# Kernel tuning notes

Measured on AMD Instinct MI355X. Metric: run time of the kernel, lower is better.

## Reference

```python
import jax, jax.numpy as jnp
import numpy as np

N_NODES = 50000
N_EDGES = 800000
IN_DIM = 128
ADD = 8
HIDDEN = 256
OUT_DIM = 128


def gcn_conv(x, src, dst, W, b, n_nodes):
    """PyG GCNConv: linear -> sym-normalized scatter-add with self-loops -> bias."""
    loop = jnp.arange(n_nodes, dtype=src.dtype)
    s = jnp.concatenate([src, loop])
    d = jnp.concatenate([dst, loop])
    deg = jax.ops.segment_sum(jnp.ones(s.shape[0], dtype=x.dtype), d, num_segments=n_nodes)
    dinv = jnp.where(deg > 0, jax.lax.rsqrt(deg), 0.0)
    norm = dinv[s] * dinv[d]                       # [E+N]
    h = x @ W                                      # [N, F_out]
    msg = h[s] * norm[:, None]                     # [E+N, F_out]
    out = jax.ops.segment_sum(msg, d, num_segments=n_nodes)
    return out + b


def prelu(x, a):
    return jnp.where(x >= 0, x, a * x)


def setup_inputs() -> dict:
    key = jax.random.key(0)
    ks = jax.random.split(key, 8)
    x = jax.random.normal(ks[0], (N_NODES, IN_DIM), dtype=jnp.float32)
    edge_index = jax.random.randint(ks[1], (2, N_EDGES), 0, N_NODES, dtype=jnp.int64)
    id_vec = jax.random.normal(ks[2], (ADD,), dtype=jnp.float32)
    # Glorot-ish init for linear weights, PReLU slope 0.25 (torch default)
    W1 = jax.random.normal(ks[3], (IN_DIM + ADD, HIDDEN), dtype=jnp.float32) * 0.05
    b1 = jnp.zeros((HIDDEN,), dtype=jnp.float32)
    a1 = jnp.full((HIDDEN,), 0.25, dtype=jnp.float32)
    W2 = jax.random.normal(ks[4], (HIDDEN, OUT_DIM), dtype=jnp.float32) * 0.05
    b2 = jnp.zeros((OUT_DIM,), dtype=jnp.float32)
    a2 = jnp.full((OUT_DIM,), 0.25, dtype=jnp.float32)
    return {"x": x, "edge_index": edge_index, "id": id_vec,
            "W1": W1, "b1": b1, "a1": a1, "W2": W2, "b2": b2, "a2": a2}


def reference(x, edge_index, id, W1, b1, a1, W2, b2, a2):
    n = x.shape[0]
    src, dst = edge_index[0], edge_index[1]
    # tile id vector onto every node and concat along features
    xi = jnp.concatenate([x, jnp.broadcast_to(id[None, :], (n, id.shape[0]))], axis=1)
    h = gcn_conv(xi, src, dst, W1, b1, n)
    h = prelu(h, a1)
    h = gcn_conv(h, src, dst, W2, b2, n)
    h = prelu(h, a2)
    return h
```

## Files before the change

kernel.cpp:

```cpp
#include <hip/hip_runtime.h>


constexpr int NN = 50000;
constexpr int NE = 800000;
constexpr int NBUCK = 98;
constexpr int TILE = 8192;
constexpr int NSCAT = (NE + TILE - 1) / TILE;

typedef __attribute__((ext_vector_type(8))) short short8;
typedef __attribute__((ext_vector_type(4))) float floatx4;

__device__ inline void bsplit(float v, unsigned short& hi, unsigned short& lo) {
  unsigned u = __float_as_uint(v);
  hi = (unsigned short)(u >> 16);
  float rem = v - __uint_as_float(u & 0xffff0000u);
  lo = (unsigned short)(__float_as_uint(rem) >> 16);
}

__device__ inline unsigned short bf16_rtne(float v) {
  unsigned u = __float_as_uint(v);
  return (unsigned short)((u + 0x7fffu + ((u >> 16) & 1u)) >> 16);
}

__device__ inline float bflo(unsigned u) { return __uint_as_float(u << 16); }
__device__ inline float bfhi(unsigned u) { return __uint_as_float(u & 0xffff0000u); }


__global__ void zero_small_kernel(int* __restrict__ bcnt) {
  int t = threadIdx.x;
  if (t < NBUCK) bcnt[t] = 0;
}

__global__ __launch_bounds__(256) void bucket_count_kernel(const int* __restrict__ ei,
                                                           int* __restrict__ bcnt) {
  __shared__ int h[NBUCK];
  int t = threadIdx.x;
  for (int i = t; i < NBUCK; i += 256) h[i] = 0;
  __syncthreads();
  int base = blockIdx.x * TILE;
  int end = base + TILE; if (end > NE) end = NE;
  for (int e = base + t; e < end; e += 256) {
    int d = ei[NE + e];
    atomicAdd(&h[d >> 9], 1);
  }
  __syncthreads();
  for (int i = t; i < NBUCK; i += 256)
    if (h[i]) atomicAdd(&bcnt[i], h[i]);
}

__global__ void bucket_scan_kernel(const int* __restrict__ bcnt, int* __restrict__ bbase,
                                   int* __restrict__ bcur) {
  __shared__ int sm[128];
  int t = threadIdx.x;
  int v = (t < NBUCK) ? bcnt[t] : 0;
  sm[t] = v;
  __syncthreads();
  for (int off = 1; off < 128; off <<= 1) {
    int u = (t >= off) ? sm[t - off] : 0;
    __syncthreads();
    sm[t] += u;
    __syncthreads();
  }
  if (t < NBUCK) {
    bbase[t] = sm[t] - v;
    bcur[t] = sm[t] - v;
  }
}

__global__ __launch_bounds__(256) void bucket_scatter_kernel(const int* __restrict__ ei,
                                                             int* __restrict__ bcur,
                                                             unsigned* __restrict__ ebuf) {
  __shared__ int h[NBUCK], lbase[NBUCK], gb[NBUCK], lcur[NBUCK];
  __shared__ int ssc[128];
  __shared__ unsigned stage[TILE];
  int t = threadIdx.x;
  for (int i = t; i < NBUCK; i += 256) h[i] = 0;
  __syncthreads();
  int base = blockIdx.x * TILE;
  int end = base + TILE; if (end > NE) end = NE;
  for (int e = base + t; e < end; e += 256) {
    int d = ei[NE + e];
    atomicAdd(&h[d >> 9], 1);
  }
  __syncthreads();
  if (t < 128) ssc[t] = (t < NBUCK) ? h[t] : 0;
  __syncthreads();
  for (int off = 1; off < 128; off <<= 1) {
    int u = 0;
    if (t < 128 && t >= off) u = ssc[t - off];
    __syncthreads();
    if (t < 128) ssc[t] += u;
    __syncthreads();
  }
  if (t < NBUCK) {
    int ex = ssc[t] - h[t];
    lbase[t] = ex;
    lcur[t] = ex;
    gb[t] = atomicAdd(&bcur[t], h[t]);
  }
  __syncthreads();
  for (int e = base + t; e < end; e += 256) {
    int s = ei[e];
    int d = ei[NE + e];
    int b = d >> 9;
    int pos = atomicAdd(&lcur[b], 1);
    stage[pos] = ((unsigned)(d & 511) << 16) | (unsigned)s;
  }
  __syncthreads();
  for (int b = 0; b < NBUCK; ++b) {
    int c = h[b], lb = lbase[b], g = gb[b];
    for (int i = t; i < c; i += 256) ebuf[g + i] = stage[lb + i];
  }
}

__global__ __launch_bounds__(256) void bucket_csr_kernel(
    const unsigned* __restrict__ ebuf, const int* __restrict__ bbase,
    const int* __restrict__ bcnt, int* __restrict__ offs, int* __restrict__ col,
    float* __restrict__ dinv) {
  __shared__ int cnt[512], cur[512], sums[256];
  int b = blockIdx.x, t = threadIdx.x;
  int node0 = b << 9;
  int nnode = NN - node0; if (nnode > 512) nnode = 512;
  for (int i = t; i < 512; i += 256) cnt[i] = 0;
  __syncthreads();
  int g0 = bbase[b], g1 = g0 + bcnt[b];
  for (int i = g0 + t; i < g1; i += 256) atomicAdd(&cnt[ebuf[i] >> 16], 1);
  __syncthreads();
  int c0 = cnt[2 * t], c1 = cnt[2 * t + 1];
  int s = c0 + c1;
  sums[t] = s;
  __syncthreads();
  for (int off = 1; off < 256; off <<= 1) {
    int u = (t >= off) ? sums[t - off] : 0;
    __syncthreads();
    sums[t] += u;
    __syncthreads();
  }
  int ex = sums[t] - s;
  cur[2 * t] = ex;
  cur[2 * t + 1] = ex + c0;
  if (2 * t < nnode) {
    offs[node0 + 2 * t] = g0 + ex;
    dinv[node0 + 2 * t] = rsqrtf((float)(c0 + 1));
  }
  if (2 * t + 1 < nnode) {
    offs[node0 + 2 * t + 1] = g0 + ex + c0;
    dinv[node0 + 2 * t + 1] = rsqrtf((float)(c1 + 1));
  }
  __syncthreads();
  for (int i = g0 + t; i < g1; i += 256) {
    unsigned v = ebuf[i];
    int dl = v >> 16;
    int pos = atomicAdd(&cur[dl], 1);
    col[g0 + pos] = (int)(v & 0xffffu);
  }
  if (b == 0 && t == 0) offs[NN] = NE;
}

__global__ void svec_kernel(const float* __restrict__ dinv, const int* __restrict__ offs,
                            const int* __restrict__ col, float* __restrict__ Svec) {
  int d = blockIdx.x * blockDim.x + threadIdx.x;
  if (d >= NN) return;
  float s = 0.f;
  int end = offs[d + 1];
  for (int p = offs[d]; p < end; ++p) s += dinv[col[p]];
  float dd = dinv[d];
  Svec[d] = dd * (dd + s);
}

__global__ void cvec_kernel(const float* __restrict__ idv, const float* __restrict__ W1,
                            float* __restrict__ cvec) {
  int m = threadIdx.x;
  float c = 0.f;
#pragma unroll
  for (int j = 0; j < 8; ++j) c += idv[j] * W1[(128 + j) * 256 + m];
  cvec[m] = c;
}

__global__ void scale_x_kernel(const float* __restrict__ x, const float* __restrict__ dinv,
                               unsigned short* __restrict__ xsb) {
  int i = blockIdx.x * blockDim.x + threadIdx.x;
  if (i < NN * 32) {
    float dd = dinv[i >> 5];
    float4 v = ((const float4*)x)[i];
    ushort4 o;
    o.x = bf16_rtne(v.x * dd);
    o.y = bf16_rtne(v.y * dd);
    o.z = bf16_rtne(v.z * dd);
    o.w = bf16_rtne(v.w * dd);
    ((ushort4*)xsb)[i] = o;
  }
}

template <int K, int N>
__global__ void pack_b_kernel(const float* __restrict__ W, unsigned short* __restrict__ Bhi,
                              unsigned short* __restrict__ Blo) {
  int id = blockIdx.x * 256 + threadIdx.x;
  if (id >= K * N) return;
  constexpr int KC = K / 32;
  int j = id & 7;
  int lane = (id >> 3) & 63;
  int rest = id >> 9;
  int c = rest % KC;
  int nt = rest / KC;
  int k = c * 32 + (lane >> 4) * 8 + j;
  int n = nt * 16 + (lane & 15);
  unsigned short hi, lo;
  bsplit(W[(size_t)k * N + n], hi, lo);
  Bhi[id] = hi;
  Blo[id] = lo;
}

template <int MODE>
__global__ __launch_bounds__(256) void agg_kernel(
    const unsigned short* __restrict__ in, const float* __restrict__ dinv,
    const int* __restrict__ offs, const int* __restrict__ col,
    const float* __restrict__ bias, const float* __restrict__ alpha,
    unsigned short* __restrict__ outhi, unsigned short* __restrict__ outlo,
    float* __restrict__ outf) {
  const uint2* inb = (const uint2*)in;
  int t = threadIdx.x;
  int node = blockIdx.x * 4 + (t >> 6);
  int lane = t & 63;
  int r = lane & 31;
  int half = lane >> 5;
  int beg = offs[node], end = offs[node + 1];

  float4 a0 = make_float4(0.f, 0.f, 0.f, 0.f);
  float4 a1 = make_float4(0.f, 0.f, 0.f, 0.f);
  int p = beg + half;
  for (; p + 6 < end; p += 8) {
    int s0 = col[p];
    int s1 = col[p + 2];
    int s2 = col[p + 4];
    int s3 = col[p + 6];
    uint2 v0 = inb[(size_t)s0 * 32 + r];
    uint2 v1 = inb[(size_t)s1 * 32 + r];
    uint2 v2 = inb[(size_t)s2 * 32 + r];
    uint2 v3 = inb[(size_t)s3 * 32 + r];
    a0.x += bflo(v0.x); a0.y += bfhi(v0.x); a0.z += bflo(v0.y); a0.w += bfhi(v0.y);
    a1.x += bflo(v1.x); a1.y += bfhi(v1.x); a1.z += bflo(v1.y); a1.w += bfhi(v1.y);
    a0.x += bflo(v2.x); a0.y += bfhi(v2.x); a0.z += bflo(v2.y); a0.w += bfhi(v2.y);
    a1.x += bflo(v3.x); a1.y += bfhi(v3.x); a1.z += bflo(v3.y); a1.w += bfhi(v3.y);
  }
  for (; p < end; p += 2) {
    uint2 v0 = inb[(size_t)col[p] * 32 + r];
    a0.x += bflo(v0.x); a0.y += bfhi(v0.x); a0.z += bflo(v0.y); a0.w += bfhi(v0.y);
  }
  float4 acc = make_float4(a0.x + a1.x, a0.y + a1.y, a0.z + a1.z, a0.w + a1.w);
  acc.x += __shfl_xor(acc.x, 32);
  acc.y += __shfl_xor(acc.y, 32);
  acc.z += __shfl_xor(acc.z, 32);
  acc.w += __shfl_xor(acc.w, 32);

  float dd = dinv[node];
  if (half == 0) {
    uint2 sv = inb[(size_t)node * 32 + r];
    acc.x = dd * (acc.x + bflo(sv.x));
    acc.y = dd * (acc.y + bfhi(sv.x));
    acc.z = dd * (acc.z + bflo(sv.y));
    acc.w = dd * (acc.w + bfhi(sv.y));
    if (MODE == 0) {
      ushort4 h4, l4;
      bsplit(acc.x, h4.x, l4.x);
      bsplit(acc.y, h4.y, l4.y);
      bsplit(acc.z, h4.z, l4.z);
      bsplit(acc.w, h4.w, l4.w);
      ((ushort4*)outhi)[(size_t)node * 32 + r] = h4;
      ((ushort4*)outlo)[(size_t)node * 32 + r] = l4;
    } else {
      float4 b = ((const float4*)bias)[r];
      float4 al = ((const float4*)alpha)[r];
      acc.x += b.x; acc.y += b.y; acc.z += b.z; acc.w += b.w;
      acc.x = (acc.x >= 0.f) ? acc.x : al.x * acc.x;
      acc.y = (acc.y >= 0.f) ? acc.y : al.y * acc.y;
      acc.z = (acc.z >= 0.f) ? acc.z : al.z * acc.z;
      acc.w = (acc.w >= 0.f) ? acc.w : al.w * acc.w;
      ((float4*)outf)[(size_t)node * 32 + r] = acc;
    }
  }
}

template <int K, int N, int MODE>
__global__ __launch_bounds__(256) void gemm_mfma_kernel(
    const unsigned short* __restrict__ Ahi, const unsigned short* __restrict__ Alo,
    const unsigned short* __restrict__ Bhi, const unsigned short* __restrict__ Blo,
    const float* __restrict__ Svec, const float* __restrict__ cvec,
    const float* __restrict__ bias, const float* __restrict__ alpha,
    const float* __restrict__ rowscale,
    unsigned short* __restrict__ Chi, unsigned short* __restrict__ Clo,
    unsigned short* __restrict__ Cb) {
  constexpr int KC = K / 32;
  constexpr int NT = N / 16;
  int wave = threadIdx.x >> 6;
  int lane = threadIdx.x & 63;
  int row0 = blockIdx.x * 64 + wave * 16;
  if (row0 >= NN) return;
  int m = lane & 15, quad = lane >> 4;
  int arow = row0 + m;

  short8 ah[KC], al[KC];
  const unsigned short* ap = Ahi + (size_t)arow * K + quad * 8;
  const unsigned short* alp = Alo + (size_t)arow * K + quad * 8;
#pragma unroll
  for (int c = 0; c < KC; ++c) {
    ah[c] = *(const short8*)(ap + c * 32);
    al[c] = *(const short8*)(alp + c * 32);
  }

  float sv[4];
#pragma unroll
  for (int i = 0; i < 4; ++i) {
    int r = row0 + quad * 4 + i;
    sv[i] = (MODE == 1) ? Svec[r] : rowscale[r];
  }

#pragma unroll 1
  for (int nt = 0; nt < NT; ++nt) {
    floatx4 acc = {0.f, 0.f, 0.f, 0.f};
#pragma unroll
    for (int c = 0; c < KC; ++c) {
      short8 bh = *(const short8*)(Bhi + ((size_t)(nt * KC + c) * 64 + lane) * 8);
      short8 bl = *(const short8*)(Blo + ((size_t)(nt * KC + c) * 64 + lane) * 8);
      acc = __builtin_amdgcn_mfma_f32_16x16x32_bf16(ah[c], bh, acc, 0, 0, 0);
      acc = __builtin_amdgcn_mfma_f32_16x16x32_bf16(ah[c], bl, acc, 0, 0, 0);
      acc = __builtin_amdgcn_mfma_f32_16x16x32_bf16(al[c], bh, acc, 0, 0, 0);
    }
    int c0 = nt * 16 + m;
    if (MODE == 1) {
      float cv = cvec[c0], bb = bias[c0], aa = alpha[c0];
#pragma unroll
      for (int i = 0; i < 4; ++i) {
        int r = row0 + quad * 4 + i;
        float v = acc[i] + sv[i] * cv + bb;
        v = (v >= 0.f) ? v : aa * v;
        unsigned short hi, lo;
        bsplit(v, hi, lo);
        Chi[(size_t)r * N + c0] = hi;
        Clo[(size_t)r * N + c0] = lo;
      }
    } else {
#pragma unroll
      for (int i = 0; i < 4; ++i) {
        int r = row0 + quad * 4 + i;
        Cb[(size_t)r * N + c0] = bf16_rtne(acc[i] * sv[i]);
      }
    }
  }
}

extern "C" void kernel_launch(void* const* d_in, const int* in_sizes, int n_in,
                              void* d_out, int out_size, void* d_ws, size_t ws_size,
                              hipStream_t stream) {
  const float* x = (const float*)d_in[0];
  const int* ei = (const int*)d_in[1];
  const float* idv = (const float*)d_in[2];
  const float* W1 = (const float*)d_in[3];
  const float* b1 = (const float*)d_in[4];
  const float* a1 = (const float*)d_in[5];
  const float* W2 = (const float*)d_in[6];
  const float* b2 = (const float*)d_in[7];
  const float* a2 = (const float*)d_in[8];
  float* out = (float*)d_out;

  char* w = (char*)d_ws;
  size_t off = 0;
  auto alloc = [&](size_t bytes) -> void* {
    void* p = w + off;
    off += bytes;
    off = (off + 255) & ~(size_t)255;
    return p;
  };
  int* bcnt = (int*)alloc((size_t)NBUCK * 4);
  int* bbase = (int*)alloc((size_t)NBUCK * 4);
  int* bcur = (int*)alloc((size_t)NBUCK * 4);
  unsigned* ebuf = (unsigned*)alloc((size_t)NE * 4);
  float* dinv = (float*)alloc((size_t)NN * 4);
  float* Svec = (float*)alloc((size_t)NN * 4);
  int* offs = (int*)alloc((size_t)(NN + 1) * 4);
  int* col = (int*)alloc((size_t)NE * 4);
  float* cvec = (float*)alloc(256 * 4);
  unsigned short* xsb = (unsigned short*)alloc((size_t)NN * 128 * 2);
  unsigned short* aggxhi = (unsigned short*)alloc((size_t)NN * 128 * 2);
  unsigned short* aggxlo = (unsigned short*)alloc((size_t)NN * 128 * 2);
  unsigned short* h1hi = (unsigned short*)alloc((size_t)NN * 256 * 2);
  unsigned short* h1lo = (unsigned short*)alloc((size_t)NN * 256 * 2);
  unsigned short* h2b = (unsigned short*)alloc((size_t)NN * 128 * 2);
  unsigned short* B1hi = (unsigned short*)alloc(128 * 256 * 2);
  unsigned short* B1lo = (unsigned short*)alloc(128 * 256 * 2);
  unsigned short* B2hi = (unsigned short*)alloc(256 * 128 * 2);
  unsigned short* B2lo = (unsigned short*)alloc(256 * 128 * 2);

  zero_small_kernel<<<1, 128, 0, stream>>>(bcnt);
  bucket_count_kernel<<<NSCAT, 256, 0, stream>>>(ei, bcnt);
  bucket_scan_kernel<<<1, 128, 0, stream>>>(bcnt, bbase, bcur);
  bucket_scatter_kernel<<<NSCAT, 256, 0, stream>>>(ei, bcur, ebuf);
  bucket_csr_kernel<<<NBUCK, 256, 0, stream>>>(ebuf, bbase, bcnt, offs, col, dinv);

  svec_kernel<<<(NN + 255) / 256, 256, 0, stream>>>(dinv, offs, col, Svec);
  cvec_kernel<<<1, 256, 0, stream>>>(idv, W1, cvec);
  scale_x_kernel<<<(NN * 32 + 255) / 256, 256, 0, stream>>>(x, dinv, xsb);
  pack_b_kernel<128, 256><<<(128 * 256 + 255) / 256, 256, 0, stream>>>(W1, B1hi, B1lo);
  pack_b_kernel<256, 128><<<(256 * 128 + 255) / 256, 256, 0, stream>>>(W2, B2hi, B2lo);

  agg_kernel<0><<<NN / 4, 256, 0, stream>>>(xsb, dinv, offs, col, nullptr, nullptr,
                                            aggxhi, aggxlo, nullptr);

  gemm_mfma_kernel<128, 256, 1><<<(NN + 63) / 64, 256, 0, stream>>>(
      aggxhi, aggxlo, B1hi, B1lo, Svec, cvec, b1, a1, nullptr, h1hi, h1lo, nullptr);

  gemm_mfma_kernel<256, 128, 2><<<(NN + 63) / 64, 256, 0, stream>>>(
      h1hi, h1lo, B2hi, B2lo, nullptr, nullptr, nullptr, nullptr, dinv,
      nullptr, nullptr, h2b);

  agg_kernel<1><<<NN / 4, 256, 0, stream>>>(h2b, dinv, offs, col, b2, a2,
                                            nullptr, nullptr, out);
}
```

Baseline: 310.0 us.

## Restructure edge bucketing with per-tile counts, smaller tiles and finer buckets

The CSR build now keeps per-tile bucket histograms and does a column-wise prefix in a single scan kernel, so the scatter kernel no longer recounts edges or takes global atomics on bucket cursors. Tiles shrink to 2048 edges, giving about 391 blocks instead of 98. Buckets narrow to 256 nodes, giving 196 CSR blocks instead of 98. The scatter write-out becomes one flat loop that uses a binary search over bucket bases. The cost is a serial scan in which each thread walks about 391 tiles, plus extra tilecnt/tpre buffers in global memory.

New measurement: 300.7 us. 1.03x faster.

```diff
diff --git a/kernel.cpp b/kernel.cpp
--- a/kernel.cpp
+++ b/kernel.cpp
@@ -3,8 +3,8 @@
 
 constexpr int NN = 50000;
 constexpr int NE = 800000;
-constexpr int NBUCK = 98;
-constexpr int TILE = 8192;
+constexpr int NBUCK = 196;
+constexpr int TILE = 2048;
 constexpr int NSCAT = (NE + TILE - 1) / TILE;
 
 typedef __attribute__((ext_vector_type(8))) short short8;
@@ -26,90 +26,87 @@
 __device__ inline float bfhi(unsigned u) { return __uint_as_float(u & 0xffff0000u); }
 
 
-__global__ void zero_small_kernel(int* __restrict__ bcnt) {
-  int t = threadIdx.x;
-  if (t < NBUCK) bcnt[t] = 0;
-}
-
-__global__ __launch_bounds__(256) void bucket_count_kernel(const int* __restrict__ ei,
-                                                           int* __restrict__ bcnt) {
+__global__ __launch_bounds__(256) void tile_count_kernel(const int* __restrict__ ei,
+                                                         int* __restrict__ tilecnt) {
   __shared__ int h[NBUCK];
   int t = threadIdx.x;
   for (int i = t; i < NBUCK; i += 256) h[i] = 0;
   __syncthreads();
   int base = blockIdx.x * TILE;
   int end = base + TILE; if (end > NE) end = NE;
-  for (int e = base + t; e < end; e += 256) {
-    int d = ei[NE + e];
-    atomicAdd(&h[d >> 9], 1);
-  }
-  __syncthreads();
-  for (int i = t; i < NBUCK; i += 256)
-    if (h[i]) atomicAdd(&bcnt[i], h[i]);
-}
-
-__global__ void bucket_scan_kernel(const int* __restrict__ bcnt, int* __restrict__ bbase,
-                                   int* __restrict__ bcur) {
-  __shared__ int sm[128];
-  int t = threadIdx.x;
-  int v = (t < NBUCK) ? bcnt[t] : 0;
-  sm[t] = v;
-  __syncthreads();
-  for (int off = 1; off < 128; off <<= 1) {
-    int u = (t >= off) ? sm[t - off] : 0;
-    __syncthreads();
-    sm[t] += u;
-    __syncthreads();
-  }
-  if (t < NBUCK) {
-    bbase[t] = sm[t] - v;
-    bcur[t] = sm[t] - v;
-  }
-}
-
-__global__ __launch_bounds__(256) void bucket_scatter_kernel(const int* __restrict__ ei,
-                                                             int* __restrict__ bcur,
-                                                             unsigned* __restrict__ ebuf) {
-  __shared__ int h[NBUCK], lbase[NBUCK], gb[NBUCK], lcur[NBUCK];
-  __shared__ int ssc[128];
+  for (int e = base + t; e < end; e += 256) atomicAdd(&h[ei[NE + e] >> 8], 1);
+  __syncthreads();
+  for (int i = t; i < NBUCK; i += 256) tilecnt[blockIdx.x * NBUCK + i] = h[i];
+}
+
+__global__ void tile_scan_kernel(const int* __restrict__ tilecnt, int* __restrict__ tpre,
+                                 int* __restrict__ bbase, int* __restrict__ bcnt) {
+  __shared__ int sums[256];
+  int b = threadIdx.x;
+  int run = 0;
+  if (b < NBUCK) {
+    for (int ti = 0; ti < NSCAT; ++ti) {
+      int idx = ti * NBUCK + b;
+      int v = tilecnt[idx];
+      tpre[idx] = run;
+      run += v;
+    }
+  }
+  sums[b] = (b < NBUCK) ? run : 0;
+  __syncthreads();
+  for (int off = 1; off < 256; off <<= 1) {
+    int u = (b >= off) ? sums[b - off] : 0;
+    __syncthreads();
+    sums[b] += u;
+    __syncthreads();
+  }
+  if (b < NBUCK) {
+    bbase[b] = sums[b] - run;
+    bcnt[b] = run;
+  }
+}
+
+__global__ __launch_bounds__(256) void bucket_scatter_kernel(
+    const int* __restrict__ ei, const int* __restrict__ tilecnt,
+    const int* __restrict__ tpre, const int* __restrict__ bbase,
+    unsigned* __restrict__ ebuf) {
+  __shared__ int lbase[NBUCK], gb[NBUCK], lcur[NBUCK], ssc[256];
   __shared__ unsigned stage[TILE];
   int t = threadIdx.x;
-  for (int i = t; i < NBUCK; i += 256) h[i] = 0;
-  __syncthreads();
-  int base = blockIdx.x * TILE;
-  int end = base + TILE; if (end > NE) end = NE;
-  for (int e = base + t; e < end; e += 256) {
-    int d = ei[NE + e];
-    atomicAdd(&h[d >> 9], 1);
-  }
-  __syncthreads();
-  if (t < 128) ssc[t] = (t < NBUCK) ? h[t] : 0;
-  __syncthreads();
-  for (int off = 1; off < 128; off <<= 1) {
-    int u = 0;
-    if (t < 128 && t >= off) u = ssc[t - off];
-    __syncthreads();
-    if (t < 128) ssc[t] += u;
+  int tile = blockIdx.x;
+  int base = tile * TILE;
+  int cntTile = NE - base; if (cntTile > TILE) cntTile = TILE;
+  int h = (t < NBUCK) ? tilecnt[tile * NBUCK + t] : 0;
+  ssc[t] = h;
+  __syncthreads();
+  for (int off = 1; off < 256; off <<= 1) {
+    int u = (t >= off) ? ssc[t - off] : 0;
+    __syncthreads();
+    ssc[t] += u;
     __syncthreads();
   }
   if (t < NBUCK) {
-    int ex = ssc[t] - h[t];
+    int ex = ssc[t] - h;
     lbase[t] = ex;
     lcur[t] = ex;
-    gb[t] = atomicAdd(&bcur[t], h[t]);
-  }
-  __syncthreads();
-  for (int e = base + t; e < end; e += 256) {
+    gb[t] = bbase[t] + tpre[tile * NBUCK + t];
+  }
+  __syncthreads();
+  for (int e = base + t; e < base + cntTile; e += 256) {
     int s = ei[e];
     int d = ei[NE + e];
-    int b = d >> 9;
+    int b = d >> 8;
     int pos = atomicAdd(&lcur[b], 1);
-    stage[pos] = ((unsigned)(d & 511) << 16) | (unsigned)s;
-  }
-  __syncthreads();
-  for (int b = 0; b < NBUCK; ++b) {
-    int c = h[b], lb = lbase[b], g = gb[b];
-    for (int i = t; i < c; i += 256) ebuf[g + i] = stage[lb + i];
+    stage[pos] = ((unsigned)(d & 255) << 16) | (unsigned)s;
+  }
+  __syncthreads();
+  for (int i = t; i < cntTile; i += 256) {
+    int lo = 0, hi = NBUCK - 1;
+    while (lo < hi) {
+      int mid = (lo + hi + 1) >> 1;
+      if (lbase[mid] <= i) lo = mid; else hi = mid - 1;
+    }
+    ebuf[gb[lo] + (i - lbase[lo])] = stage[i];
   }
 }
 
@@ -117,18 +114,16 @@
     const unsigned* __restrict__ ebuf, const int* __restrict__ bbase,
     const int* __restrict__ bcnt, int* __restrict__ offs, int* __restrict__ col,
     float* __restrict__ dinv) {
-  __shared__ int cnt[512], cur[512], sums[256];
+  __shared__ int cnt[256], cur[256], sums[256];
   int b = blockIdx.x, t = threadIdx.x;
-  int node0 = b << 9;
-  int nnode = NN - node0; if (nnode > 512) nnode = 512;
-  for (int i = t; i < 512; i += 256) cnt[i] = 0;
+  int node0 = b << 8;
+  cnt[t] = 0;
   __syncthreads();
   int g0 = bbase[b], g1 = g0 + bcnt[b];
   for (int i = g0 + t; i < g1; i += 256) atomicAdd(&cnt[ebuf[i] >> 16], 1);
   __syncthreads();
-  int c0 = cnt[2 * t], c1 = cnt[2 * t + 1];
-  int s = c0 + c1;
-  sums[t] = s;
+  int c = cnt[t];
+  sums[t] = c;
   __syncthreads();
   for (int off = 1; off < 256; off <<= 1) {
     int u = (t >= off) ? sums[t - off] : 0;
@@ -136,22 +131,17 @@
     sums[t] += u;
     __syncthreads();
   }
-  int ex = sums[t] - s;
-  cur[2 * t] = ex;
-  cur[2 * t + 1] = ex + c0;
-  if (2 * t < nnode) {
-    offs[node0 + 2 * t] = g0 + ex;
-    dinv[node0 + 2 * t] = rsqrtf((float)(c0 + 1));
-  }
-  if (2 * t + 1 < nnode) {
-    offs[node0 + 2 * t + 1] = g0 + ex + c0;
-    dinv[node0 + 2 * t + 1] = rsqrtf((float)(c1 + 1));
+  int ex = sums[t] - c;
+  cur[t] = ex;
+  int node = node0 + t;
+  if (node < NN) {
+    offs[node] = g0 + ex;
+    dinv[node] = rsqrtf((float)(c + 1));
   }
   __syncthreads();
   for (int i = g0 + t; i < g1; i += 256) {
     unsigned v = ebuf[i];
-    int dl = v >> 16;
-    int pos = atomicAdd(&cur[dl], 1);
+    int pos = atomicAdd(&cur[v >> 16], 1);
     col[g0 + pos] = (int)(v & 0xffffu);
   }
   if (b == 0 && t == 0) offs[NN] = NE;
@@ -371,9 +361,10 @@
     off = (off + 255) & ~(size_t)255;
     return p;
   };
+  int* tilecnt = (int*)alloc((size_t)NSCAT * NBUCK * 4);
+  int* tpre = (int*)alloc((size_t)NSCAT * NBUCK * 4);
+  int* bbase = (int*)alloc((size_t)NBUCK * 4);
   int* bcnt = (int*)alloc((size_t)NBUCK * 4);
-  int* bbase = (int*)alloc((size_t)NBUCK * 4);
-  int* bcur = (int*)alloc((size_t)NBUCK * 4);
   unsigned* ebuf = (unsigned*)alloc((size_t)NE * 4);
   float* dinv = (float*)alloc((size_t)NN * 4);
   float* Svec = (float*)alloc((size_t)NN * 4);
@@ -391,10 +382,9 @@
   unsigned short* B2hi = (unsigned short*)alloc(256 * 128 * 2);
   unsigned short* B2lo = (unsigned short*)alloc(256 * 128 * 2);
 
-  zero_small_kernel<<<1, 128, 0, stream>>>(bcnt);
-  bucket_count_kernel<<<NSCAT, 256, 0, stream>>>(ei, bcnt);
-  bucket_scan_kernel<<<1, 128, 0, stream>>>(bcnt, bbase, bcur);
-  bucket_scatter_kernel<<<NSCAT, 256, 0, stream>>>(ei, bcur, ebuf);
+  tile_count_kernel<<<NSCAT, 256, 0, stream>>>(ei, tilecnt);
+  tile_scan_kernel<<<1, 256, 0, stream>>>(tilecnt, tpre, bbase, bcnt);
+  bucket_scatter_kernel<<<NSCAT, 256, 0, stream>>>(ei, tilecnt, tpre, bbase, ebuf);
   bucket_csr_kernel<<<NBUCK, 256, 0, stream>>>(ebuf, bbase, bcnt, offs, col, dinv);
 
   svec_kernel<<<(NN + 255) / 256, 256, 0, stream>>>(dinv, offs, col, Svec);
```
